# Performance work log

Hardware: AMD Instinct MI355X
Metric: run time of the kernel (lower is better)

Reference implementation:

```python
import jax, jax.numpy as jnp
import numpy as np

B, N, DIN, DOUT = 2048, 64, 512, 512


def setup_inputs() -> dict:
    key = jax.random.key(0)
    kx, kw, kb = jax.random.split(key, 3)
    x = jax.random.normal(kx, (B, N, DIN), dtype=jnp.float32)
    # stacked per-node Linear params (PyTorch Linear: y = x @ W.T + b)
    bound = 1.0 / np.sqrt(DIN)
    W = jax.random.uniform(kw, (N, DIN, DOUT), dtype=jnp.float32, minval=-bound, maxval=bound)
    b = jax.random.uniform(kb, (N, DOUT), dtype=jnp.float32, minval=-bound, maxval=bound)
    return {"x": x, "W": W, "b": b}


def reference(x, W, b):
    # per-node independent linear layers fused into one batched GEMM
    # x: [B, N, DIN], W: [N, DIN, DOUT], b: [N, DOUT]
    y = jnp.einsum('bni,nio->bno', x, W) + b  # [B, N, DOUT]
    # torch.cat along dim=1 of the per-node [B, DOUT] outputs == flatten node axis
    return y.reshape(x.shape[0], -1)  # [B, N*DOUT]
```

## Files before the change

kernel.cpp:

```cpp
#include <hip/hip_runtime.h>


#define NN 64
#define DIN 512
#define DOUT 512
#define BM 128
#define BN 256
#define BK 32
#define KSTEPS (DIN / BK)
#define ROWSTRIDE (NN * DIN)
#define OUTSTRIDE (NN * DOUT)

typedef __bf16 bf16x8 __attribute__((ext_vector_type(8)));
typedef float f32x4 __attribute__((ext_vector_type(4)));

__device__ __forceinline__ unsigned short f2bf(float f) {
    return __builtin_bit_cast(unsigned short, (__bf16)f);
}
__device__ __forceinline__ unsigned int f2bf2(float a, float b) {
    return (unsigned int)f2bf(a) | ((unsigned int)f2bf(b) << 16);
}

typedef const __attribute__((address_space(1))) unsigned int* gas1_t;
typedef __attribute__((address_space(3))) unsigned int* las3_t;
__device__ __forceinline__ void gload_lds16(const void* g, void* l) {
    __builtin_amdgcn_global_load_lds((gas1_t)g, (las3_t)l, 16, 0, 0);
}

#define WAITV(n)  asm volatile("s_waitcnt vmcnt(" #n ")" ::: "memory")
#define WAITLGKM  asm volatile("s_waitcnt lgkmcnt(0)" ::: "memory")

__global__ void wt_transpose_kernel(const float* __restrict__ W,
                                    unsigned short* __restrict__ Wt) {
    __shared__ float tile[32][33];
    const int n  = blockIdx.z;
    const int i0 = blockIdx.x * 32;
    const int o0 = blockIdx.y * 32;
    const float* Wn = W + (size_t)n * DIN * DOUT;
    unsigned short* Wtn = Wt + (size_t)n * DIN * DOUT;
    const int tx = threadIdx.x, ty = threadIdx.y;
#pragma unroll
    for (int q = 0; q < 4; ++q)
        tile[ty + q * 8][tx] = Wn[(size_t)(i0 + ty + q * 8) * DOUT + (o0 + tx)];
    __syncthreads();
#pragma unroll
    for (int q = 0; q < 4; ++q)
        Wtn[(size_t)(o0 + ty + q * 8) * DIN + (i0 + tx)] = f2bf(tile[tx][ty + q * 8]);
}

__global__ __launch_bounds__(512, 4) void node_gemm_kernel(
    const float* __restrict__ X, const unsigned short* __restrict__ Wt,
    const float* __restrict__ Bias, float* __restrict__ Out) {
    __shared__ unsigned short As[2][BM * BK];
    __shared__ unsigned short Bs[2][BN * BK];

    const int bid = blockIdx.x;
    const int swz = (bid & 7) * 256 + (bid >> 3);
    const int node  = swz >> 5;
    const int rem   = swz & 31;
    const int mtile = rem >> 1;
    const int ntile = rem & 1;
    const int brow = mtile * BM;
    const int bcol = ntile * BN;

    const int tid  = threadIdx.x;
    const int lane = tid & 63;
    const int w    = tid >> 6;
    const int wm   = w >> 2;
    const int wn   = w & 3;

    const float* Xb = X + (size_t)brow * ROWSTRIDE + node * DIN;
    const unsigned short* Wb = Wt + (size_t)node * DIN * DOUT + (size_t)bcol * DIN;

    const int a_r  = tid >> 2;
    const int a_s  = tid & 3;
    const int a_sw = a_s ^ ((a_r >> 1) & 3);
    const float* a_src = Xb + (size_t)a_r * ROWSTRIDE + a_s * 8;
    const int a_dst = a_r * BK + a_sw * 8;

    const unsigned short* b_src[2];
    int b_dst[2];
#pragma unroll
    for (int q = 0; q < 2; ++q) {
        const int i = q * 8 + w;
        const int c = i * 16 + (lane >> 2);
        const int s = lane & 3;
        const int gs = s ^ ((c >> 1) & 3);
        b_src[q] = Wb + (size_t)c * DIN + gs * 8;
        b_dst[q] = i * 512;
    }

    const int arow = lane & 15;
    const int akk  = lane >> 4;
    const int kswz = akk ^ ((arow >> 1) & 3);
    const int afrag = (wm * 64 + arow) * BK + kswz * 8;
    const int bfrag = (wn * 64 + arow) * BK + kswz * 8;

    f32x4 acc[4][4] = {};
    float4 av0, av1;

    auto stageB = [&](int buf, int kt) {
#pragma unroll
        for (int q = 0; q < 2; ++q)
            gload_lds16(b_src[q] + kt * BK, &Bs[buf][b_dst[q]]);
    };
    auto loadA = [&](int kt) {
        const float* p = a_src + kt * BK;
        av0 = *reinterpret_cast<const float4*>(p);
        av1 = *reinterpret_cast<const float4*>(p + 4);
    };
    auto storeA = [&](int buf) {
        uint4 pk;
        pk.x = f2bf2(av0.x, av0.y);
        pk.y = f2bf2(av0.z, av0.w);
        pk.z = f2bf2(av1.x, av1.y);
        pk.w = f2bf2(av1.z, av1.w);
        *reinterpret_cast<uint4*>(&As[buf][a_dst]) = pk;
    };
    auto compute = [&](int buf) {
        bf16x8 af[4], bq[4];
#pragma unroll
        for (int m = 0; m < 4; ++m)
            af[m] = *reinterpret_cast<const bf16x8*>(&As[buf][afrag + m * 16 * BK]);
#pragma unroll
        for (int n = 0; n < 4; ++n)
            bq[n] = *reinterpret_cast<const bf16x8*>(&Bs[buf][bfrag + n * 16 * BK]);
        __builtin_amdgcn_s_setprio(1);
#pragma unroll
        for (int m = 0; m < 4; ++m)
#pragma unroll
            for (int n = 0; n < 4; ++n)
                acc[m][n] = __builtin_amdgcn_mfma_f32_16x16x32_bf16(af[m], bq[n], acc[m][n], 0, 0, 0);
        __builtin_amdgcn_s_setprio(0);
    };

    loadA(0);
    stageB(0, 0);
    WAITV(2);
    storeA(0);
    WAITLGKM;
    __builtin_amdgcn_s_barrier();

#pragma unroll
    for (int kt = 0; kt < KSTEPS; ++kt) {
        const int buf = kt & 1;
        if (kt + 1 < KSTEPS) {
            loadA(kt + 1);
            stageB(buf ^ 1, kt + 1);
            WAITV(4);
        } else {
            WAITV(0);
        }
        compute(buf);
        if (kt + 1 < KSTEPS) {
            WAITV(2);
            storeA(buf ^ 1);
            WAITLGKM;
            __builtin_amdgcn_s_barrier();
        }
    }

    const float* bn = Bias + node * DOUT + bcol;
    float* outb = Out + (size_t)brow * OUTSTRIDE + node * DOUT + bcol;
#pragma unroll
    for (int n = 0; n < 4; ++n) {
        const int col = wn * 64 + n * 16 + arow;
        const float bias = bn[col];
#pragma unroll
        for (int m = 0; m < 4; ++m) {
            const int r0 = wm * 64 + m * 16 + akk * 4;
#pragma unroll
            for (int j = 0; j < 4; ++j)
                outb[(size_t)(r0 + j) * OUTSTRIDE + col] = acc[m][n][j] + bias;
        }
    }
}

extern "C" void kernel_launch(void* const* d_in, const int* in_sizes, int n_in,
                              void* d_out, int out_size, void* d_ws, size_t ws_size,
                              hipStream_t stream) {
    const float* x = (const float*)d_in[0];
    const float* W = (const float*)d_in[1];
    const float* b = (const float*)d_in[2];
    float* out = (float*)d_out;
    unsigned short* Wt = (unsigned short*)d_ws;

    wt_transpose_kernel<<<dim3(DIN / 32, DOUT / 32, NN), dim3(32, 8), 0, stream>>>(W, Wt);
    node_gemm_kernel<<<dim3(2048), dim3(512), 0, stream>>>(x, Wt, b, out);
}
```

Measured before the change: 203.1 us.

## Enlarge GEMM tiles to 256x256x64 with pre-swizzled panelized weight layout

```diff
diff --git a/kernel.cpp b/kernel.cpp
--- a/kernel.cpp
+++ b/kernel.cpp
@@ -4,12 +4,13 @@
 #define NN 64
 #define DIN 512
 #define DOUT 512
-#define BM 128
+#define BM 256
 #define BN 256
-#define BK 32
-#define KSTEPS (DIN / BK)
+#define BK 64
+#define NTILES 8
 #define ROWSTRIDE (NN * DIN)
 #define OUTSTRIDE (NN * DOUT)
+#define PANEL 16384
 
 typedef __bf16 bf16x8 __attribute__((ext_vector_type(8)));
 typedef float f32x4 __attribute__((ext_vector_type(4)));
@@ -31,37 +32,43 @@
 #define WAITLGKM  asm volatile("s_waitcnt lgkmcnt(0)" ::: "memory")
 
 __global__ void wt_transpose_kernel(const float* __restrict__ W,
-                                    unsigned short* __restrict__ Wt) {
+                                    unsigned short* __restrict__ Wt2) {
     __shared__ float tile[32][33];
     const int n  = blockIdx.z;
     const int i0 = blockIdx.x * 32;
     const int o0 = blockIdx.y * 32;
     const float* Wn = W + (size_t)n * DIN * DOUT;
-    unsigned short* Wtn = Wt + (size_t)n * DIN * DOUT;
     const int tx = threadIdx.x, ty = threadIdx.y;
 #pragma unroll
     for (int q = 0; q < 4; ++q)
         tile[ty + q * 8][tx] = Wn[(size_t)(i0 + ty + q * 8) * DOUT + (o0 + tx)];
     __syncthreads();
 #pragma unroll
-    for (int q = 0; q < 4; ++q)
-        Wtn[(size_t)(o0 + ty + q * 8) * DIN + (i0 + tx)] = f2bf(tile[tx][ty + q * 8]);
-}
-
-__global__ __launch_bounds__(512, 4) void node_gemm_kernel(
-    const float* __restrict__ X, const unsigned short* __restrict__ Wt,
+    for (int q = 0; q < 4; ++q) {
+        const int o = o0 + ty + q * 8;
+        const int i = i0 + tx;
+        const int nt = o >> 8, col = o & 255;
+        const int kt = i >> 6, slot = (i >> 3) & 7, e = i & 7;
+        const size_t idx = ((size_t)((n * 2 + nt) * 8 + kt)) * PANEL +
+                           col * 64 + ((slot ^ (col & 7)) * 8) + e;
+        Wt2[idx] = f2bf(tile[tx][ty + q * 8]);
+    }
+}
+
+__global__ __launch_bounds__(512, 2) void node_gemm_kernel(
+    const float* __restrict__ X, const unsigned short* __restrict__ Wt2,
     const float* __restrict__ Bias, float* __restrict__ Out) {
-    __shared__ unsigned short As[2][BM * BK];
-    __shared__ unsigned short Bs[2][BN * BK];
-
-    const int bid = blockIdx.x;
-    const int swz = (bid & 7) * 256 + (bid >> 3);
-    const int node  = swz >> 5;
-    const int rem   = swz & 31;
+    __shared__ unsigned short As[2][BM * 64];
+    __shared__ unsigned short Bs[2][BN * 64];
+
+    const int bid  = blockIdx.x;
+    const int xcd  = bid & 7;
+    const int seq  = bid >> 3;
+    const int node = (seq >> 4) * 8 + xcd;
+    const int rem  = seq & 15;
     const int mtile = rem >> 1;
     const int ntile = rem & 1;
     const int brow = mtile * BM;
-    const int bcol = ntile * BN;
 
     const int tid  = threadIdx.x;
     const int lane = tid & 63;
@@ -70,105 +77,111 @@
     const int wn   = w & 3;
 
     const float* Xb = X + (size_t)brow * ROWSTRIDE + node * DIN;
-    const unsigned short* Wb = Wt + (size_t)node * DIN * DOUT + (size_t)bcol * DIN;
-
-    const int a_r  = tid >> 2;
-    const int a_s  = tid & 3;
-    const int a_sw = a_s ^ ((a_r >> 1) & 3);
-    const float* a_src = Xb + (size_t)a_r * ROWSTRIDE + a_s * 8;
-    const int a_dst = a_r * BK + a_sw * 8;
-
-    const unsigned short* b_src[2];
-    int b_dst[2];
-#pragma unroll
-    for (int q = 0; q < 2; ++q) {
-        const int i = q * 8 + w;
-        const int c = i * 16 + (lane >> 2);
-        const int s = lane & 3;
-        const int gs = s ^ ((c >> 1) & 3);
-        b_src[q] = Wb + (size_t)c * DIN + gs * 8;
-        b_dst[q] = i * 512;
-    }
-
-    const int arow = lane & 15;
+    const unsigned short* Wb2 = Wt2 + (size_t)((node * 2 + ntile) * 8) * PANEL;
+
+    const int a_row  = tid >> 1;
+    const int a_half = tid & 1;
+    const float* a_src = Xb + (size_t)a_row * ROWSTRIDE + a_half * 32;
+    const int a_base = a_row * 64;
+    const int a_rx   = a_row & 7;
+
+    const int frow = lane & 15;
     const int akk  = lane >> 4;
-    const int kswz = akk ^ ((arow >> 1) & 3);
-    const int afrag = (wm * 64 + arow) * BK + kswz * 8;
-    const int bfrag = (wn * 64 + arow) * BK + kswz * 8;
-
-    f32x4 acc[4][4] = {};
-    float4 av0, av1;
-
-    auto stageB = [&](int buf, int kt) {
-#pragma unroll
-        for (int q = 0; q < 2; ++q)
-            gload_lds16(b_src[q] + kt * BK, &Bs[buf][b_dst[q]]);
-    };
+    const int cx   = frow & 7;
+
+    f32x4 acc[8][4] = {};
+    float4 av[8];
+
     auto loadA = [&](int kt) {
         const float* p = a_src + kt * BK;
-        av0 = *reinterpret_cast<const float4*>(p);
-        av1 = *reinterpret_cast<const float4*>(p + 4);
+#pragma unroll
+        for (int i = 0; i < 8; ++i)
+            av[i] = *reinterpret_cast<const float4*>(p + i * 4);
     };
     auto storeA = [&](int buf) {
-        uint4 pk;
-        pk.x = f2bf2(av0.x, av0.y);
-        pk.y = f2bf2(av0.z, av0.w);
-        pk.z = f2bf2(av1.x, av1.y);
-        pk.w = f2bf2(av1.z, av1.w);
-        *reinterpret_cast<uint4*>(&As[buf][a_dst]) = pk;
+#pragma unroll
+        for (int j = 0; j < 4; ++j) {
+            uint4 pk;
+            pk.x = f2bf2(av[2 * j].x, av[2 * j].y);
+            pk.y = f2bf2(av[2 * j].z, av[2 * j].w);
+            pk.z = f2bf2(av[2 * j + 1].x, av[2 * j + 1].y);
+            pk.w = f2bf2(av[2 * j + 1].z, av[2 * j + 1].w);
+            *reinterpret_cast<uint4*>(
+                &As[buf][a_base + ((a_half * 4 + j) ^ a_rx) * 8]) = pk;
+        }
+    };
+    auto stageB = [&](int buf, int kt) {
+#pragma unroll
+        for (int q = 0; q < 4; ++q) {
+            const int c = w * 4 + q;
+            gload_lds16(Wb2 + (size_t)kt * PANEL + c * 512 + lane * 8,
+                        &Bs[buf][c * 512]);
+        }
     };
     auto compute = [&](int buf) {
-        bf16x8 af[4], bq[4];
-#pragma unroll
-        for (int m = 0; m < 4; ++m)
-            af[m] = *reinterpret_cast<const bf16x8*>(&As[buf][afrag + m * 16 * BK]);
-#pragma unroll
-        for (int n = 0; n < 4; ++n)
-            bq[n] = *reinterpret_cast<const bf16x8*>(&Bs[buf][bfrag + n * 16 * BK]);
-        __builtin_amdgcn_s_setprio(1);
-#pragma unroll
-        for (int m = 0; m < 4; ++m)
+#pragma unroll
+        for (int kk = 0; kk < 2; ++kk) {
+            const int ks = ((kk * 4 + akk) ^ cx) * 8;
+            bf16x8 bq[4];
 #pragma unroll
             for (int n = 0; n < 4; ++n)
-                acc[m][n] = __builtin_amdgcn_mfma_f32_16x16x32_bf16(af[m], bq[n], acc[m][n], 0, 0, 0);
-        __builtin_amdgcn_s_setprio(0);
+                bq[n] = *reinterpret_cast<const bf16x8*>(
+                    &Bs[buf][(wn * 64 + n * 16 + frow) * 64 + ks]);
+#pragma unroll
+            for (int mh = 0; mh < 2; ++mh) {
+                bf16x8 af[4];
+#pragma unroll
+                for (int m = 0; m < 4; ++m)
+                    af[m] = *reinterpret_cast<const bf16x8*>(
+                        &As[buf][(wm * 128 + (mh * 4 + m) * 16 + frow) * 64 + ks]);
+                __builtin_amdgcn_s_setprio(1);
+#pragma unroll
+                for (int m = 0; m < 4; ++m)
+#pragma unroll
+                    for (int n = 0; n < 4; ++n)
+                        acc[mh * 4 + m][n] = __builtin_amdgcn_mfma_f32_16x16x32_bf16(
+                            af[m], bq[n], acc[mh * 4 + m][n], 0, 0, 0);
+                __builtin_amdgcn_s_setprio(0);
+            }
+        }
     };
 
     loadA(0);
+    WAITV(0);
+    storeA(0);
     stageB(0, 0);
-    WAITV(2);
-    storeA(0);
-    WAITLGKM;
-    __builtin_amdgcn_s_barrier();
-
-#pragma unroll
-    for (int kt = 0; kt < KSTEPS; ++kt) {
-        const int buf = kt & 1;
-        if (kt + 1 < KSTEPS) {
-            loadA(kt + 1);
-            stageB(buf ^ 1, kt + 1);
-            WAITV(4);
+
+#pragma unroll
+    for (int t = 0; t < NTILES; ++t) {
+        const int buf = t & 1;
+        WAITLGKM;
+        __builtin_amdgcn_s_barrier();
+        __builtin_amdgcn_sched_barrier(0);
+        if (t < NTILES - 1) {
+            loadA(t + 1);
+            stageB(buf ^ 1, t + 1);
+            WAITV(12);
         } else {
             WAITV(0);
         }
+        __builtin_amdgcn_sched_barrier(0);
         compute(buf);
-        if (kt + 1 < KSTEPS) {
-            WAITV(2);
+        if (t < NTILES - 1) {
+            WAITV(4);
+            __builtin_amdgcn_sched_barrier(0);
             storeA(buf ^ 1);
-            WAITLGKM;
-            __builtin_amdgcn_s_barrier();
         }
     }
 
-    const float* bn = Bias + node * DOUT + bcol;
-    float* outb = Out + (size_t)brow * OUTSTRIDE + node * DOUT + bcol;
+    const float* bn = Bias + node * DOUT + ntile * 256;
+    float* outb = Out + (size_t)brow * OUTSTRIDE + node * DOUT + ntile * 256;
 #pragma unroll
     for (int n = 0; n < 4; ++n) {
-        const int col = wn * 64 + n * 16 + arow;
+        const int col = wn * 64 + n * 16 + frow;
         const float bias = bn[col];
 #pragma unroll
-        for (int m = 0; m < 4; ++m) {
-            const int r0 = wm * 64 + m * 16 + akk * 4;
+        for (int m = 0; m < 8; ++m) {
+            const int r0 = wm * 128 + m * 16 + akk * 4;
 #pragma unroll
             for (int j = 0; j < 4; ++j)
                 outb[(size_t)(r0 + j) * OUTSTRIDE + col] = acc[m][n][j] + bias;
@@ -183,8 +196,8 @@
     const float* W = (const float*)d_in[1];
     const float* b = (const float*)d_in[2];
     float* out = (float*)d_out;
-    unsigned short* Wt = (unsigned short*)d_ws;
-
-    wt_transpose_kernel<<<dim3(DIN / 32, DOUT / 32, NN), dim3(32, 8), 0, stream>>>(W, Wt);
-    node_gemm_kernel<<<dim3(2048), dim3(512), 0, stream>>>(x, Wt, b, out);
-}
+    unsigned short* Wt2 = (unsigned short*)d_ws;
+
+    wt_transpose_kernel<<<dim3(DIN / 32, DOUT / 32, NN), dim3(32, 8), 0, stream>>>(W, Wt2);
+    node_gemm_kernel<<<dim3(1024), dim3(512), 0, stream>>>(x, Wt2, b, out);
+}
```

After: 253.3 us (median of 5 runs). +24.7%, slower.
